# Kernel optimization log

Hardware: AMD Instinct MI355X
Metric: run time of the kernel (lower is better)

The kernel has to match this reference:

```python
import jax, jax.numpy as jnp
import numpy as np

W_SEG = 2048   # segment_length w
R = 4          # dilation r
H = 16         # num_attention_heads


def setup_inputs() -> dict:
    key = jax.random.key(0)
    k0, k1, k2 = jax.random.split(key, 3)
    B, S, Hid = 2, 8192, 1024
    X = jax.random.normal(k0, (B, S, Hid), dtype=jnp.float32)
    Wq = jax.random.normal(k1, (Hid, Hid), dtype=jnp.float32) * 0.02
    bq = jnp.zeros((Hid,), jnp.float32)
    Wkv = jax.random.normal(k2, (Hid, 2 * Hid), dtype=jnp.float32) * 0.02
    bkv = jnp.zeros((2 * Hid,), jnp.float32)
    return {"X": X, "Wq": Wq, "bq": bq, "Wkv": Wkv, "bkv": bkv}


def reference(X, Wq, bq, Wkv, bkv):
    B, S, Hid = X.shape
    D = Hid // H                      # head dim
    num_points = W_SEG // R           # tokens kept per segment
    num_seg = S // W_SEG
    scale = 1.0 / np.sqrt(D).astype(np.float32)

    q = (X @ Wq + bq).reshape(B, S, H, D)
    kv = (X @ Wkv + bkv).reshape(B, S, 2, H, D)
    k, v = kv[:, :, 0], kv[:, :, 1]

    # dilated base indices: segment offset + r-strided points -> [num_seg*num_points]
    base = (jnp.arange(num_seg)[:, None] * W_SEG
            + jnp.arange(num_points)[None, :] * R).reshape(-1)
    shift = jnp.arange(H) % R                       # per-head shift
    idx = base[None, :] + shift[:, None]            # [H, T']
    Tq = idx.shape[1]
    idxT = idx.T                                    # [T', H]
    head_ix = jnp.arange(H)[None, :]                # [1, H] -> broadcasts with idxT

    # per-head dilated gather: sparse[b, t, h, d] = full[b, idx[h, t], h, d]
    sq = q[:, idxT, head_ix, :]                     # [B, T', H, D]
    sk = k[:, idxT, head_ix, :]
    sv = v[:, idxT, head_ix, :]

    sq = sq.reshape(B, num_seg, num_points, H, D)
    sk = sk.reshape(B, num_seg, num_points, H, D)
    sv = sv.reshape(B, num_seg, num_points, H, D)

    # per-segment (non-causal) attention, same math as flash_attn_kvpacked_func
    scores = jnp.einsum('bsqhd,bskhd->bshqk', sq, sk) * scale
    probs = jax.nn.softmax(scores, axis=-1)
    ctx = jnp.einsum('bshqk,bskhd->bsqhd', probs, sv)
    ctx = ctx.reshape(B, Tq, H, D)

    # scatter back into zeros at the gathered positions (unique per head)
    out = jnp.zeros((B, S, H, D), ctx.dtype).at[:, idxT, head_ix, :].set(ctx)
    return out.reshape(B, S, Hid)
```

## Files before the change

### kernel.cpp

```cpp
#include <hip/hip_runtime.h>

typedef unsigned short u16;
typedef unsigned int   u32;
typedef __bf16 bf16x8 __attribute__((ext_vector_type(8)));
typedef float  f32x4  __attribute__((ext_vector_type(4)));
typedef short  s16x4  __attribute__((ext_vector_type(4)));

#define QSCALE 0.125f

__device__ __forceinline__ u16 f2bf(float f) {
  union { float f; u32 u; } a; a.f = f;
  u32 u = a.u;
  u = (u + 0x7FFFu + ((u >> 16) & 1u)) >> 16;
  return (u16)u;
}

__device__ __forceinline__ void async16(const void* g, void* l) {
  __builtin_amdgcn_global_load_lds(
      (const __attribute__((address_space(1))) void*)g,
      (__attribute__((address_space(3))) void*)l, 16, 0, 0);
}

__global__ __launch_bounds__(256) void pack_x(const float* __restrict__ X,
                                              u16* __restrict__ Xp) {
  __shared__ uint4 lds[2048];
  int bx  = blockIdx.x;
  int ks4 = bx & 7;
  int Mt  = (bx >> 3) & 31;
  int r   = bx >> 8;
  int bseg = Mt >> 2;
  int p0   = (Mt & 3) * 128;
  int tid = threadIdx.x;
  int lane16 = tid & 15;
  int r16    = tid >> 4;
  int ksl = lane16 >> 2, kc = lane16 & 3;
  int xsw = (ksl * 4 + kc) & 7;
#pragma unroll
  for (int it = 0; it < 8; ++it) {
    int m_local = it * 16 + r16;
    const float* src = X + (size_t)(bseg * 2048 + (p0 + m_local) * 4 + r) * 1024
                         + ks4 * 128 + lane16 * 8;
    float4 v0 = *(const float4*)src;
    float4 v1 = *(const float4*)(src + 4);
    uint4 o;
    o.x = f2bf(v0.x) | ((u32)f2bf(v0.y) << 16);
    o.y = f2bf(v0.z) | ((u32)f2bf(v0.w) << 16);
    o.z = f2bf(v1.x) | ((u32)f2bf(v1.y) << 16);
    o.w = f2bf(v1.z) | ((u32)f2bf(v1.w) << 16);
    lds[ksl * 512 + it * 64 + kc * 16 + (r16 ^ xsw)] = o;
  }
  __syncthreads();
  u16* outb = Xp + (size_t)r * 4194304 + (size_t)Mt * 131072 + (size_t)ks4 * 16384;
#pragma unroll
  for (int jt = 0; jt < 8; ++jt) {
    int g = jt * 256 + tid;
    int ksl2 = g >> 9, v = g & 511;
    int kc2 = (v >> 4) & 3, mm2 = v & 15;
    uint4 o = lds[ksl2 * 512 + (v & ~15) + (mm2 ^ ((ksl2 * 4 + kc2) & 7))];
    *(uint4*)(outb + (size_t)g * 8) = o;
  }
}

__global__ __launch_bounds__(256) void pack_w(const float* __restrict__ Wq,
                                              const float* __restrict__ Wkv,
                                              u16* __restrict__ Wp,
                                              const float* __restrict__ bq,
                                              const float* __restrict__ bkv,
                                              float* __restrict__ bp) {
  __shared__ float tile[32][65];
  int bx = blockIdx.x;
  if (bx >= 1536) {
    int idx = (bx - 1536) * 256 + threadIdx.x;
    int r = idx / 768, n = idx % 768;
    int t = n >> 8, hh = (n >> 6) & 3, d = n & 63;
    int h = hh * 4 + r;
    float v = (t == 0) ? bq[h * 64 + d] * QSCALE
            : (t == 1) ? bkv[h * 64 + d]
                       : bkv[1024 + h * 64 + d];
    bp[idx] = v;
    return;
  }
  int ks = bx & 31; int rem = bx >> 5;
  int hh = rem & 3; rem >>= 2;
  int t  = rem % 3; int r = rem / 3;
  int h  = hh * 4 + r;
  const float* src; int rs, cb;
  if (t == 0)      { src = Wq;  rs = 1024; cb = h * 64; }
  else if (t == 1) { src = Wkv; rs = 2048; cb = h * 64; }
  else             { src = Wkv; rs = 2048; cb = 1024 + h * 64; }
  int tid = threadIdx.x;
  {
    int kk = tid >> 3, dd = (tid & 7) << 3;
    const float* s0 = src + (size_t)(ks * 32 + kk) * rs + cb + dd;
    float4 a = *(const float4*)s0;
    float4 c = *(const float4*)(s0 + 4);
    tile[kk][dd + 0] = a.x; tile[kk][dd + 1] = a.y;
    tile[kk][dd + 2] = a.z; tile[kk][dd + 3] = a.w;
    tile[kk][dd + 4] = c.x; tile[kk][dd + 5] = c.y;
    tile[kk][dd + 6] = c.z; tile[kk][dd + 7] = c.w;
  }
  __syncthreads();
  {
    int d = tid >> 2, kc = tid & 3;
    float sc = (t == 0) ? QSCALE : 1.0f;
    u32 w[4];
#pragma unroll
    for (int j = 0; j < 4; ++j) {
      u16 lo = f2bf(tile[kc * 8 + 2 * j][d] * sc);
      u16 hi = f2bf(tile[kc * 8 + 2 * j + 1][d] * sc);
      w[j] = (u32)lo | ((u32)hi << 16);
    }
    int n = t * 256 + hh * 64 + d;
    int Nt = n >> 7, nt = (n >> 4) & 7, nn = n & 15;
    size_t off = (size_t)r * 786432 + (size_t)Nt * 131072 +
                 (size_t)ks * 4096 + nt * 512 + kc * 128 + nn * 8;
    uint4 o; o.x = w[0]; o.y = w[1]; o.z = w[2]; o.w = w[3];
    *(uint4*)(Wp + off) = o;
  }
}

__global__ __launch_bounds__(256, 3) void gemm1(const u16* __restrict__ Xp,
                                                const u16* __restrict__ Wp,
                                                const float* __restrict__ bp,
                                                u16* __restrict__ Qd,
                                                u16* __restrict__ Kd,
                                                u16* __restrict__ Vd) {
  __shared__ u16 ldsAB[8192];
  u16* ldsA = ldsAB;
  u16* ldsB = ldsAB + 4096;
  int bx = blockIdx.x;
  int xcd = bx & 7;
  int idx = bx >> 3;
  int r = xcd >> 1;
  int Mtile = (xcd & 1) * 16 + (idx / 6);
  int Ntile = idx % 6;
  int tid = threadIdx.x, w = tid >> 6, lane = tid & 63;
  int wr = w >> 1, wc = w & 1;
  int l15 = lane & 15, l4 = lane >> 4;

  const u16* Asrc = Xp + (size_t)r * 4194304 + (size_t)Mtile * 131072 +
                    w * 1024 + lane * 8;
  const u16* Bsrc = Wp + (size_t)r * 786432 + (size_t)Ntile * 131072 +
                    w * 1024 + lane * 8;

  f32x4 acc[4][4] = {};
  for (int ks = 0; ks < 32; ++ks) {
    const u16* a = Asrc + ks * 4096;
    const u16* b = Bsrc + ks * 4096;
    async16(a,       &ldsA[w * 1024]);
    async16(a + 512, &ldsA[w * 1024 + 512]);
    async16(b,       &ldsB[w * 1024]);
    async16(b + 512, &ldsB[w * 1024 + 512]);
    __syncthreads();
    bf16x8 af[4], bf[4];
#pragma unroll
    for (int i = 0; i < 4; ++i)
      af[i] = *(const bf16x8*)&ldsA[((wr * 4 + i) * 64 + lane) * 8];
#pragma unroll
    for (int j = 0; j < 4; ++j)
      bf[j] = *(const bf16x8*)&ldsB[((wc * 4 + j) * 64 + lane) * 8];
#pragma unroll
    for (int i = 0; i < 4; ++i)
#pragma unroll
      for (int j = 0; j < 4; ++j)
        acc[i][j] = __builtin_amdgcn_mfma_f32_16x16x32_bf16(af[i], bf[j],
                                                            acc[i][j], 0, 0, 0);
    __syncthreads();
  }

  int nb = Ntile * 128 + wc * 64;
  int t = nb >> 8, hh = (nb >> 6) & 3;
  int h = hh * 4 + r;
  u16* T = (t == 0) ? Qd : ((t == 1) ? Kd : Vd);
  float biasv[4];
#pragma unroll
  for (int j = 0; j < 4; ++j) biasv[j] = bp[r * 768 + nb + j * 16 + l15];

  u16* eb = ldsAB + w * 1152;
  int rrow = lane >> 2, seg = lane & 3;
#pragma unroll
  for (int i = 0; i < 4; ++i) {
    __syncthreads();
#pragma unroll
    for (int j = 0; j < 4; ++j)
#pragma unroll
      for (int reg = 0; reg < 4; ++reg)
        eb[(l4 * 4 + reg) * 72 + j * 16 + l15] = f2bf(acc[i][j][reg] + biasv[j]);
    __syncthreads();
    uint4 d0 = *(const uint4*)&eb[rrow * 72 + seg * 16];
    uint4 d1 = *(const uint4*)&eb[rrow * 72 + seg * 16 + 8];
    int m = Mtile * 128 + wr * 64 + i * 16 + rrow;
    int bseg = m >> 9, p = m & 511;
    size_t off = ((size_t)(bseg * 16 + h) * 512 + p) * 64 + seg * 16;
    *(uint4*)(T + off) = d0;
    *(uint4*)(T + off + 8) = d1;
  }
}

__global__ __launch_bounds__(512, 4) void attn(const u16* __restrict__ Qd,
                                               const u16* __restrict__ Kd,
                                               const u16* __restrict__ Vd,
                                               float* __restrict__ out) {
  __shared__ u16 ldsK[128 * 72];
  __shared__ u16 ldsV[64 * 136];
  int bx = blockIdx.x;
  int unit = bx & 127, qq = bx >> 7;
  int b = unit >> 6, seg = (unit >> 4) & 3, h = unit & 15;
  int tid = threadIdx.x, w = tid >> 6, lane = tid & 63;
  int l15 = lane & 15, l4 = lane >> 4;
  const u16* Qu = Qd + (size_t)unit * 32768;
  const u16* Ku = Kd + (size_t)unit * 32768;
  const u16* Vu = Vd + (size_t)unit * 32768;

  int q0 = qq * 128 + w * 16;
  bf16x8 qf[2];
#pragma unroll
  for (int hf = 0; hf < 2; ++hf)
    qf[hf] = *(const bf16x8*)(Qu + (q0 + l15) * 64 + hf * 32 + l4 * 8);

  f32x4 O[4] = {};
  float lrun = 0.f;

  int c0 = tid, c1 = 512 + tid;
  int kp0 = c0 >> 3, kd0 = c0 & 7;
  int kp1 = c1 >> 3, kd1 = c1 & 7;
  int vd0 = (c0 & 7) << 3, vd1 = (c1 & 7) << 3;

  uint4 kreg0 = *(const uint4*)(Ku + c0 * 8);
  uint4 kreg1 = *(const uint4*)(Ku + c1 * 8);
  uint4 vreg0 = *(const uint4*)(Vu + c0 * 8);
  uint4 vreg1 = *(const uint4*)(Vu + c1 * 8);

  for (int ch = 0; ch < 4; ++ch) {
    __syncthreads();
    *(uint4*)&ldsK[kp0 * 72 + kd0 * 8] = kreg0;
    *(uint4*)&ldsK[kp1 * 72 + kd1 * 8] = kreg1;
    {
      u32 ww0[4] = {vreg0.x, vreg0.y, vreg0.z, vreg0.w};
      u32 ww1[4] = {vreg1.x, vreg1.y, vreg1.z, vreg1.w};
#pragma unroll
      for (int j = 0; j < 4; ++j) {
        ldsV[(vd0 + 2 * j) * 136 + kp0]     = (u16)(ww0[j] & 0xFFFFu);
        ldsV[(vd0 + 2 * j + 1) * 136 + kp0] = (u16)(ww0[j] >> 16);
        ldsV[(vd1 + 2 * j) * 136 + kp1]     = (u16)(ww1[j] & 0xFFFFu);
        ldsV[(vd1 + 2 * j + 1) * 136 + kp1] = (u16)(ww1[j] >> 16);
      }
    }
    __syncthreads();
    if (ch < 3) {
      const u16* Ksn = Ku + (ch + 1) * 8192;
      const u16* Vsn = Vu + (ch + 1) * 8192;
      kreg0 = *(const uint4*)(Ksn + c0 * 8);
      kreg1 = *(const uint4*)(Ksn + c1 * 8);
      vreg0 = *(const uint4*)(Vsn + c0 * 8);
      vreg1 = *(const uint4*)(Vsn + c1 * 8);
    }

    float csum = 0.f;
    s16x4 pk[8];
#pragma unroll
    for (int kt = 0; kt < 8; ++kt) {
      bf16x8 a0 = *(const bf16x8*)&ldsK[(kt * 16 + l15) * 72 + l4 * 8];
      bf16x8 a1 = *(const bf16x8*)&ldsK[(kt * 16 + l15) * 72 + 32 + l4 * 8];
      f32x4 s = __builtin_amdgcn_mfma_f32_16x16x32_bf16(
          a0, qf[0], (f32x4){0.f, 0.f, 0.f, 0.f}, 0, 0, 0);
      s = __builtin_amdgcn_mfma_f32_16x16x32_bf16(a1, qf[1], s, 0, 0, 0);
      float e0 = __expf(s[0]);
      float e1 = __expf(s[1]);
      float e2 = __expf(s[2]);
      float e3 = __expf(s[3]);
      csum += (e0 + e1) + (e2 + e3);
      s16x4 pv;
      pv[0] = (short)(__float_as_uint(e0) >> 16);
      pv[1] = (short)(__float_as_uint(e1) >> 16);
      pv[2] = (short)(__float_as_uint(e2) >> 16);
      pv[3] = (short)(__float_as_uint(e3) >> 16);
      pk[kt] = pv;
    }
    csum += __shfl_xor(csum, 16, 64);
    csum += __shfl_xor(csum, 32, 64);
    lrun += csum;
#pragma unroll
    for (int kt = 0; kt < 8; ++kt)
#pragma unroll
      for (int dn = 0; dn < 4; ++dn) {
        s16x4 vb = *(const s16x4*)&ldsV[(dn * 16 + l15) * 136 + kt * 16 + l4 * 4];
        O[dn] = __builtin_amdgcn_mfma_f32_16x16x16bf16_1k(pk[kt], vb,
                                                          O[dn], 0, 0, 0);
      }
  }

  {
    float rl = __builtin_amdgcn_rcpf(lrun);
#pragma unroll
    for (int reg = 0; reg < 4; ++reg) {
      float rr = __shfl(rl, l4 * 4 + reg, 64);
      int p = q0 + l4 * 4 + reg;
      int spos = seg * 2048 + p * 4 + (h & 3);
      size_t base = ((size_t)(b * 8192 + spos)) * 1024 + h * 64 + l15;
#pragma unroll
      for (int dn = 0; dn < 4; ++dn)
        out[base + dn * 16] = O[dn][reg] * rr;
    }
  }

  {
    int row_i = bx * 32 + (tid >> 4);
    int sub = tid & 15;
    int rr = row_i & 3;
    float4 z = {0.f, 0.f, 0.f, 0.f};
    float* rowp = out + (size_t)row_i * 1024 + sub * 4;
#pragma unroll
    for (int hz = 0; hz < 16; ++hz) {
      if ((hz & 3) == rr) continue;
      *(float4*)(rowp + hz * 64) = z;
    }
  }
}

extern "C" void kernel_launch(void* const* d_in, const int* in_sizes, int n_in,
                              void* d_out, int out_size, void* d_ws, size_t ws_size,
                              hipStream_t stream) {
  (void)in_sizes; (void)n_in; (void)ws_size; (void)out_size;
  const float* X   = (const float*)d_in[0];
  const float* Wq  = (const float*)d_in[1];
  const float* bq  = (const float*)d_in[2];
  const float* Wkv = (const float*)d_in[3];
  const float* bkv = (const float*)d_in[4];
  float* out = (float*)d_out;
  char* ws = (char*)d_ws;
  u16*  Xp = (u16*)(ws);
  u16*  Wp = (u16*)(ws + 33554432);
  float* bp = (float*)(ws + 39845888);
  u16*  Qd = (u16*)(ws + 39858176);
  u16*  Kd = (u16*)(ws + 48246784);
  u16*  Vd = (u16*)(ws + 56635392);

  pack_x <<<1024, 256, 0, stream>>>(X, Xp);
  pack_w <<<1548, 256, 0, stream>>>(Wq, Wkv, Wp, bq, bkv, bp);
  gemm1  <<<768,  256, 0, stream>>>(Xp, Wp, bp, Qd, Kd, Vd);
  attn   <<<512,  512, 0, stream>>>(Qd, Kd, Vd, out);
}
```

Before: 197.5 us.

## Fuse X fp32-to-bf16 packing into projection GEMM and drop pack_x kernel

Removes the separate pack_x kernel and has gemm1 read fp32 X directly, converting it to bf16 in registers (round-half-up via add+perm) and storing to LDS, with the next k-step's X prefetched into registers. This drops a 32 MB workspace write and reread plus a kernel launch. In exchange each of the 6 N-tile blocks rereads the fp32 X rows (twice the bytes per read), rounding changes from round-to-nearest-even to round-half-up, and one barrier per iteration is removed by reordering the syncs.

```diff
diff --git a/kernel.cpp b/kernel.cpp
--- a/kernel.cpp
+++ b/kernel.cpp
@@ -19,46 +19,6 @@
   __builtin_amdgcn_global_load_lds(
       (const __attribute__((address_space(1))) void*)g,
       (__attribute__((address_space(3))) void*)l, 16, 0, 0);
-}
-
-__global__ __launch_bounds__(256) void pack_x(const float* __restrict__ X,
-                                              u16* __restrict__ Xp) {
-  __shared__ uint4 lds[2048];
-  int bx  = blockIdx.x;
-  int ks4 = bx & 7;
-  int Mt  = (bx >> 3) & 31;
-  int r   = bx >> 8;
-  int bseg = Mt >> 2;
-  int p0   = (Mt & 3) * 128;
-  int tid = threadIdx.x;
-  int lane16 = tid & 15;
-  int r16    = tid >> 4;
-  int ksl = lane16 >> 2, kc = lane16 & 3;
-  int xsw = (ksl * 4 + kc) & 7;
-#pragma unroll
-  for (int it = 0; it < 8; ++it) {
-    int m_local = it * 16 + r16;
-    const float* src = X + (size_t)(bseg * 2048 + (p0 + m_local) * 4 + r) * 1024
-                         + ks4 * 128 + lane16 * 8;
-    float4 v0 = *(const float4*)src;
-    float4 v1 = *(const float4*)(src + 4);
-    uint4 o;
-    o.x = f2bf(v0.x) | ((u32)f2bf(v0.y) << 16);
-    o.y = f2bf(v0.z) | ((u32)f2bf(v0.w) << 16);
-    o.z = f2bf(v1.x) | ((u32)f2bf(v1.y) << 16);
-    o.w = f2bf(v1.z) | ((u32)f2bf(v1.w) << 16);
-    lds[ksl * 512 + it * 64 + kc * 16 + (r16 ^ xsw)] = o;
-  }
-  __syncthreads();
-  u16* outb = Xp + (size_t)r * 4194304 + (size_t)Mt * 131072 + (size_t)ks4 * 16384;
-#pragma unroll
-  for (int jt = 0; jt < 8; ++jt) {
-    int g = jt * 256 + tid;
-    int ksl2 = g >> 9, v = g & 511;
-    int kc2 = (v >> 4) & 3, mm2 = v & 15;
-    uint4 o = lds[ksl2 * 512 + (v & ~15) + (mm2 ^ ((ksl2 * 4 + kc2) & 7))];
-    *(uint4*)(outb + (size_t)g * 8) = o;
-  }
 }
 
 __global__ __launch_bounds__(256) void pack_w(const float* __restrict__ Wq,
@@ -119,7 +79,7 @@
   }
 }
 
-__global__ __launch_bounds__(256, 3) void gemm1(const u16* __restrict__ Xp,
+__global__ __launch_bounds__(256, 3) void gemm1(const float* __restrict__ X,
                                                 const u16* __restrict__ Wp,
                                                 const float* __restrict__ bp,
                                                 u16* __restrict__ Qd,
@@ -138,19 +98,40 @@
   int wr = w >> 1, wc = w & 1;
   int l15 = lane & 15, l4 = lane >> 4;
 
-  const u16* Asrc = Xp + (size_t)r * 4194304 + (size_t)Mtile * 131072 +
-                    w * 1024 + lane * 8;
+  int rl = tid >> 1, tq = tid & 1;
+  int srow = (Mtile >> 2) * 2048 + ((Mtile & 3) * 128 + rl) * 4 + r;
+  const float* Xthr = X + (size_t)srow * 1024 + tq * 4;
+  int abase = ((rl >> 4) * 64 + (rl & 15)) * 8 + tq * 4;
+
   const u16* Bsrc = Wp + (size_t)r * 786432 + (size_t)Ntile * 131072 +
                     w * 1024 + lane * 8;
 
+  float4 ar[4];
+#pragma unroll
+  for (int it = 0; it < 4; ++it) ar[it] = *(const float4*)(Xthr + it * 8);
+
   f32x4 acc[4][4] = {};
   for (int ks = 0; ks < 32; ++ks) {
-    const u16* a = Asrc + ks * 4096;
+    __syncthreads();
+#pragma unroll
+    for (int it = 0; it < 4; ++it) {
+      u32 x0 = __float_as_uint(ar[it].x) + 0x8000u;
+      u32 x1 = __float_as_uint(ar[it].y) + 0x8000u;
+      u32 x2 = __float_as_uint(ar[it].z) + 0x8000u;
+      u32 x3 = __float_as_uint(ar[it].w) + 0x8000u;
+      u32 lo = __builtin_amdgcn_perm(x1, x0, 0x07060302u);
+      u32 hi = __builtin_amdgcn_perm(x3, x2, 0x07060302u);
+      uint2 d2; d2.x = lo; d2.y = hi;
+      *(uint2*)&ldsA[abase + it * 128] = d2;
+    }
     const u16* b = Bsrc + ks * 4096;
-    async16(a,       &ldsA[w * 1024]);
-    async16(a + 512, &ldsA[w * 1024 + 512]);
     async16(b,       &ldsB[w * 1024]);
     async16(b + 512, &ldsB[w * 1024 + 512]);
+    if (ks < 31) {
+      const float* xn = Xthr + (ks + 1) * 32;
+#pragma unroll
+      for (int it = 0; it < 4; ++it) ar[it] = *(const float4*)(xn + it * 8);
+    }
     __syncthreads();
     bf16x8 af[4], bf[4];
 #pragma unroll
@@ -165,7 +146,6 @@
       for (int j = 0; j < 4; ++j)
         acc[i][j] = __builtin_amdgcn_mfma_f32_16x16x32_bf16(af[i], bf[j],
                                                             acc[i][j], 0, 0, 0);
-    __syncthreads();
   }
 
   int nb = Ntile * 128 + wc * 64;
@@ -329,15 +309,13 @@
   const float* bkv = (const float*)d_in[4];
   float* out = (float*)d_out;
   char* ws = (char*)d_ws;
-  u16*  Xp = (u16*)(ws);
-  u16*  Wp = (u16*)(ws + 33554432);
-  float* bp = (float*)(ws + 39845888);
-  u16*  Qd = (u16*)(ws + 39858176);
-  u16*  Kd = (u16*)(ws + 48246784);
-  u16*  Vd = (u16*)(ws + 56635392);
-
-  pack_x <<<1024, 256, 0, stream>>>(X, Xp);
+  u16*  Wp = (u16*)(ws);
+  float* bp = (float*)(ws + 6291456);
+  u16*  Qd = (u16*)(ws + 6303744);
+  u16*  Kd = (u16*)(ws + 14692352);
+  u16*  Vd = (u16*)(ws + 23080960);
+
   pack_w <<<1548, 256, 0, stream>>>(Wq, Wkv, Wp, bq, bkv, bp);
-  gemm1  <<<768,  256, 0, stream>>>(Xp, Wp, bp, Qd, Kd, Vd);
+  gemm1  <<<768,  256, 0, stream>>>(X, Wp, bp, Qd, Kd, Vd);
   attn   <<<512,  512, 0, stream>>>(Qd, Kd, Vd, out);
 }
```

New measurement: 187.6 us. -5.0%, faster.
